# Performance work log

Hardware: AMD Instinct MI355X
Metric: run time of the kernel (lower is better)

Reference implementation:

```python
import jax, jax.numpy as jnp
from jax import lax
import numpy as np

TAPS = 4          # db2 filter length
LEVEL = 4
CH = 32
SLOPE = 10.0      # sigmoid sharpness of learned hard-threshold activation

# db2 decomposition low-pass coefficients (pywt convention)
_DB2 = np.array([-0.12940952255126037, 0.2241438680420134,
                 0.8365163037378079, 0.48296291314453416], dtype=np.float32)

def setup_inputs() -> dict:
    key = jax.random.key(0)
    k1, k2, k3 = jax.random.split(key, 3)
    x = jax.random.normal(k1, (128, CH, 4096), dtype=jnp.float32)
    # learned per-channel, per-level low-pass kernels: db2 init + small perturbation
    h_lo = jnp.asarray(_DB2)[None, None, :] + 0.02 * jax.random.normal(
        k2, (CH, LEVEL, TAPS), dtype=jnp.float32)
    # learned symmetric thresholds (Act_Init=0 -> small positive values)
    bias = 0.1 * jax.random.uniform(k3, (CH, LEVEL), dtype=jnp.float32)
    return {"x": x, "h_lo": h_lo, "bias": bias}

def _grouped_dwt_step(a, k_lo, k_hi):
    # a: [B,C,T]; kernels: [C,1,taps]; circular boundary, stride-2 downsample
    B, C, T = a.shape
    a_pad = jnp.concatenate([a, a[..., : TAPS - 1]], axis=-1)  # circular pad
    dn = ('NCH', 'OIH', 'NCH')
    lo = lax.conv_general_dilated(a_pad, k_lo, (2,), 'VALID',
                                  dimension_numbers=dn, feature_group_count=C)
    hi = lax.conv_general_dilated(a_pad, k_hi, (2,), 'VALID',
                                  dimension_numbers=dn, feature_group_count=C)
    return lo, hi  # each [B,C,T//2]

def reference(x, h_lo, bias):
    """Batched learned wavelet decomposition (all channels at once via grouped conv).
    Returns coefficients packed along last dim: [yl, d_L, ..., d_1] -> [B,C,T].
    """
    B, C, T = x.shape
    sign = ((-1.0) ** jnp.arange(TAPS)).astype(x.dtype)  # QMF sign flip
    a = x
    details = []
    for l in range(LEVEL):
        k_lo = h_lo[:, l, :][:, None, :]                       # [C,1,taps]
        k_hi = (sign * h_lo[:, l, ::-1])[:, None, :]           # high-pass via QMF
        a, hi = _grouped_dwt_step(a, k_lo, k_hi)
        b = bias[None, :, l, None]                             # [1,C,1]
        # symmetric sigmoid (soft hard-threshold) activation on detail coeffs
        d = hi * (jax.nn.sigmoid(SLOPE * (hi - b)) + jax.nn.sigmoid(-SLOPE * (hi + b)))
        details.append(d)
    # pack: approximation (coarsest) first, then details coarsest->finest
    return jnp.concatenate([a] + details[::-1], axis=-1)
```

## Files before the change

### kernel.cpp

```cpp
#include <hip/hip_runtime.h>
#include <math.h>

#define TLEN 4096
#define LEVELS 4
#define CHANS 32
#define SLOPE 10.0f

__device__ __forceinline__ float clamp30(float v) {
    return __builtin_amdgcn_fmed3f(v, -30.f, 30.f);
}

__device__ __forceinline__ float sgate(float hi, float b) {
    const float ea = __expf(clamp30(-SLOPE * (hi - b)));
    const float eb = __expf(clamp30( SLOPE * (hi + b)));
    return hi * (2.f + ea + eb) * __builtin_amdgcn_rcpf((1.f + ea) * (1.f + eb));
}

__global__ __launch_bounds__(256) void lwpt_kernel(
    const float* __restrict__ x, const float* __restrict__ h_lo,
    const float* __restrict__ bias, float* __restrict__ out)
{
    __shared__ float bufA[2048];
    __shared__ float bufB[1024];

    const int bc  = blockIdx.x;
    const int c   = bc & (CHANS - 1);
    const int tid = threadIdx.x;

    const float* xrow = x   + (size_t)bc * TLEN;
    float*       orow = out + (size_t)bc * TLEN;

    const float4 k0v = ((const float4*)h_lo)[c * LEVELS + 0];
    const float4 k1v = ((const float4*)h_lo)[c * LEVELS + 1];
    const float4 k2v = ((const float4*)h_lo)[c * LEVELS + 2];
    const float4 k3v = ((const float4*)h_lo)[c * LEVELS + 3];
    const float b0 = bias[c * LEVELS + 0];
    const float b1 = bias[c * LEVELS + 1];
    const float b2 = bias[c * LEVELS + 2];
    const float b3 = bias[c * LEVELS + 3];

    {
        const float4* x4 = (const float4*)xrow;
        float in[18];
        #pragma unroll
        for (int k = 0; k < 4; ++k) {
            const float4 v = x4[4 * tid + k];
            in[4*k+0] = v.x; in[4*k+1] = v.y; in[4*k+2] = v.z; in[4*k+3] = v.w;
        }
        const float2 e = *(const float2*)(xrow + ((16 * tid + 16) & (TLEN - 1)));
        in[16] = e.x; in[17] = e.y;

        float lo[8], dd[8];
        #pragma unroll
        for (int j = 0; j < 8; ++j) {
            const float a0 = in[2*j], a1 = in[2*j+1], a2 = in[2*j+2], a3 = in[2*j+3];
            lo[j] = a0*k0v.x + a1*k0v.y + a2*k0v.z + a3*k0v.w;
            const float hi = a0*k0v.w - a1*k0v.z + a2*k0v.y - a3*k0v.x;
            dd[j] = sgate(hi, b0);
        }
        ((float4*)bufA)[tid]          = make_float4(lo[0], lo[1], lo[2], lo[3]);
        ((float4*)(bufA + 1024))[tid] = make_float4(lo[4], lo[5], lo[6], lo[7]);
        float4* o4 = (float4*)(orow + 2048);
        o4[2*tid]   = make_float4(dd[0], dd[1], dd[2], dd[3]);
        o4[2*tid+1] = make_float4(dd[4], dd[5], dd[6], dd[7]);
    }
    __syncthreads();

    {
        float in[10];
        const float4 v0 = ((const float4*)bufA)[tid];
        const float4 v1 = ((const float4*)(bufA + 1024))[tid];
        in[0] = v0.x; in[1] = v0.y; in[2] = v0.z; in[3] = v0.w;
        in[4] = v1.x; in[5] = v1.y; in[6] = v1.z; in[7] = v1.w;
        const float2 e = *(const float2*)(bufA + ((4 * (tid + 1)) & 1023));
        in[8] = e.x; in[9] = e.y;

        float lo[4], dd[4];
        #pragma unroll
        for (int j = 0; j < 4; ++j) {
            const float a0 = in[2*j], a1 = in[2*j+1], a2 = in[2*j+2], a3 = in[2*j+3];
            lo[j] = a0*k1v.x + a1*k1v.y + a2*k1v.z + a3*k1v.w;
            const float hi = a0*k1v.w - a1*k1v.z + a2*k1v.y - a3*k1v.x;
            dd[j] = sgate(hi, b1);
        }
        ((float4*)bufB)[tid] = make_float4(lo[0], lo[1], lo[2], lo[3]);
        ((float4*)(orow + 1024))[tid] = make_float4(dd[0], dd[1], dd[2], dd[3]);
    }
    __syncthreads();

    {
        float in[6];
        const float4 v = ((const float4*)bufB)[tid];
        in[0] = v.x; in[1] = v.y; in[2] = v.z; in[3] = v.w;
        const float2 e = *(const float2*)(bufB + ((4 * tid + 4) & 1023));
        in[4] = e.x; in[5] = e.y;

        float lo[2], dd[2];
        #pragma unroll
        for (int j = 0; j < 2; ++j) {
            const float a0 = in[2*j], a1 = in[2*j+1], a2 = in[2*j+2], a3 = in[2*j+3];
            lo[j] = a0*k2v.x + a1*k2v.y + a2*k2v.z + a3*k2v.w;
            const float hi = a0*k2v.w - a1*k2v.z + a2*k2v.y - a3*k2v.x;
            dd[j] = sgate(hi, b2);
        }
        ((float2*)bufA)[tid] = make_float2(lo[0], lo[1]);
        ((float2*)(orow + 512))[tid] = make_float2(dd[0], dd[1]);
    }
    __syncthreads();

    {
        const float2 a01 = *(const float2*)(bufA + 2 * tid);
        const float2 e   = *(const float2*)(bufA + ((2 * tid + 2) & 511));
        const float a0 = a01.x, a1 = a01.y, a2 = e.x, a3 = e.y;
        const float lo = a0*k3v.x + a1*k3v.y + a2*k3v.z + a3*k3v.w;
        const float hi = a0*k3v.w - a1*k3v.z + a2*k3v.y - a3*k3v.x;
        orow[tid]       = lo;
        orow[256 + tid] = sgate(hi, b3);
    }
}

extern "C" void kernel_launch(void* const* d_in, const int* in_sizes, int n_in,
                              void* d_out, int out_size, void* d_ws, size_t ws_size,
                              hipStream_t stream) {
    const float* x    = (const float*)d_in[0];
    const float* h_lo = (const float*)d_in[1];
    const float* bias = (const float*)d_in[2];
    float* out = (float*)d_out;

    dim3 grid(128 * CHANS);
    dim3 block(256);
    lwpt_kernel<<<grid, block, 0, stream>>>(x, h_lo, bias, out);
}
```

Before: 26.29 us.

## Replace shared-memory level exchange with per-thread halo recomputation

Each thread now loads a wider input window (46 samples including a 30-sample halo) and computes all four wavelet levels entirely in registers. This removes the LDS buffers and the three block barriers between levels. In exchange it recomputes overlapping low-pass outputs (22 instead of 8 at level one, and so on), issues extra global loads that overlap with neighbouring threads, and raises register use.

Result: slower. 29.14 us (+10.8%).

```diff
diff --git a/kernel.cpp b/kernel.cpp
--- a/kernel.cpp
+++ b/kernel.cpp
@@ -20,9 +20,6 @@
     const float* __restrict__ x, const float* __restrict__ h_lo,
     const float* __restrict__ bias, float* __restrict__ out)
 {
-    __shared__ float bufA[2048];
-    __shared__ float bufB[1024];
-
     const int bc  = blockIdx.x;
     const int c   = bc & (CHANS - 1);
     const int tid = threadIdx.x;
@@ -39,81 +36,70 @@
     const float b2 = bias[c * LEVELS + 2];
     const float b3 = bias[c * LEVELS + 3];
 
+    float in[46];
+    const int base = 16 * tid;
+    #pragma unroll
+    for (int k = 0; k < 4; ++k) {
+        const float4 v = *(const float4*)(xrow + base + 4 * k);
+        in[4*k+0] = v.x; in[4*k+1] = v.y; in[4*k+2] = v.z; in[4*k+3] = v.w;
+    }
+    #pragma unroll
+    for (int k = 0; k < 7; ++k) {
+        const float4 v = *(const float4*)(xrow + ((base + 16 + 4 * k) & (TLEN - 1)));
+        in[16+4*k+0] = v.x; in[16+4*k+1] = v.y; in[16+4*k+2] = v.z; in[16+4*k+3] = v.w;
+    }
     {
-        const float4* x4 = (const float4*)xrow;
-        float in[18];
-        #pragma unroll
-        for (int k = 0; k < 4; ++k) {
-            const float4 v = x4[4 * tid + k];
-            in[4*k+0] = v.x; in[4*k+1] = v.y; in[4*k+2] = v.z; in[4*k+3] = v.w;
-        }
-        const float2 e = *(const float2*)(xrow + ((16 * tid + 16) & (TLEN - 1)));
-        in[16] = e.x; in[17] = e.y;
+        const float2 e = *(const float2*)(xrow + ((base + 44) & (TLEN - 1)));
+        in[44] = e.x; in[45] = e.y;
+    }
 
-        float lo[8], dd[8];
+    float lo1[22];
+    #pragma unroll
+    for (int j = 0; j < 22; ++j)
+        lo1[j] = in[2*j]*k0v.x + in[2*j+1]*k0v.y + in[2*j+2]*k0v.z + in[2*j+3]*k0v.w;
+    {
+        float dd[8];
         #pragma unroll
         for (int j = 0; j < 8; ++j) {
-            const float a0 = in[2*j], a1 = in[2*j+1], a2 = in[2*j+2], a3 = in[2*j+3];
-            lo[j] = a0*k0v.x + a1*k0v.y + a2*k0v.z + a3*k0v.w;
-            const float hi = a0*k0v.w - a1*k0v.z + a2*k0v.y - a3*k0v.x;
+            const float hi = in[2*j]*k0v.w - in[2*j+1]*k0v.z + in[2*j+2]*k0v.y - in[2*j+3]*k0v.x;
             dd[j] = sgate(hi, b0);
         }
-        ((float4*)bufA)[tid]          = make_float4(lo[0], lo[1], lo[2], lo[3]);
-        ((float4*)(bufA + 1024))[tid] = make_float4(lo[4], lo[5], lo[6], lo[7]);
         float4* o4 = (float4*)(orow + 2048);
         o4[2*tid]   = make_float4(dd[0], dd[1], dd[2], dd[3]);
         o4[2*tid+1] = make_float4(dd[4], dd[5], dd[6], dd[7]);
     }
-    __syncthreads();
+
+    float lo2[10];
+    #pragma unroll
+    for (int j = 0; j < 10; ++j)
+        lo2[j] = lo1[2*j]*k1v.x + lo1[2*j+1]*k1v.y + lo1[2*j+2]*k1v.z + lo1[2*j+3]*k1v.w;
+    {
+        float dd[4];
+        #pragma unroll
+        for (int j = 0; j < 4; ++j) {
+            const float hi = lo1[2*j]*k1v.w - lo1[2*j+1]*k1v.z + lo1[2*j+2]*k1v.y - lo1[2*j+3]*k1v.x;
+            dd[j] = sgate(hi, b1);
+        }
+        ((float4*)(orow + 1024))[tid] = make_float4(dd[0], dd[1], dd[2], dd[3]);
+    }
+
+    float lo3[4];
+    #pragma unroll
+    for (int j = 0; j < 4; ++j)
+        lo3[j] = lo2[2*j]*k2v.x + lo2[2*j+1]*k2v.y + lo2[2*j+2]*k2v.z + lo2[2*j+3]*k2v.w;
+    {
+        float dd[2];
+        #pragma unroll
+        for (int j = 0; j < 2; ++j) {
+            const float hi = lo2[2*j]*k2v.w - lo2[2*j+1]*k2v.z + lo2[2*j+2]*k2v.y - lo2[2*j+3]*k2v.x;
+            dd[j] = sgate(hi, b2);
+        }
+        ((float2*)(orow + 512))[tid] = make_float2(dd[0], dd[1]);
+    }
 
     {
-        float in[10];
-        const float4 v0 = ((const float4*)bufA)[tid];
-        const float4 v1 = ((const float4*)(bufA + 1024))[tid];
-        in[0] = v0.x; in[1] = v0.y; in[2] = v0.z; in[3] = v0.w;
-        in[4] = v1.x; in[5] = v1.y; in[6] = v1.z; in[7] = v1.w;
-        const float2 e = *(const float2*)(bufA + ((4 * (tid + 1)) & 1023));
-        in[8] = e.x; in[9] = e.y;
-
-        float lo[4], dd[4];
-        #pragma unroll
-        for (int j = 0; j < 4; ++j) {
-            const float a0 = in[2*j], a1 = in[2*j+1], a2 = in[2*j+2], a3 = in[2*j+3];
-            lo[j] = a0*k1v.x + a1*k1v.y + a2*k1v.z + a3*k1v.w;
-            const float hi = a0*k1v.w - a1*k1v.z + a2*k1v.y - a3*k1v.x;
-            dd[j] = sgate(hi, b1);
-        }
-        ((float4*)bufB)[tid] = make_float4(lo[0], lo[1], lo[2], lo[3]);
-        ((float4*)(orow + 1024))[tid] = make_float4(dd[0], dd[1], dd[2], dd[3]);
-    }
-    __syncthreads();
-
-    {
-        float in[6];
-        const float4 v = ((const float4*)bufB)[tid];
-        in[0] = v.x; in[1] = v.y; in[2] = v.z; in[3] = v.w;
-        const float2 e = *(const float2*)(bufB + ((4 * tid + 4) & 1023));
-        in[4] = e.x; in[5] = e.y;
-
-        float lo[2], dd[2];
-        #pragma unroll
-        for (int j = 0; j < 2; ++j) {
-            const float a0 = in[2*j], a1 = in[2*j+1], a2 = in[2*j+2], a3 = in[2*j+3];
-            lo[j] = a0*k2v.x + a1*k2v.y + a2*k2v.z + a3*k2v.w;
-            const float hi = a0*k2v.w - a1*k2v.z + a2*k2v.y - a3*k2v.x;
-            dd[j] = sgate(hi, b2);
-        }
-        ((float2*)bufA)[tid] = make_float2(lo[0], lo[1]);
-        ((float2*)(orow + 512))[tid] = make_float2(dd[0], dd[1]);
-    }
-    __syncthreads();
-
-    {
-        const float2 a01 = *(const float2*)(bufA + 2 * tid);
-        const float2 e   = *(const float2*)(bufA + ((2 * tid + 2) & 511));
-        const float a0 = a01.x, a1 = a01.y, a2 = e.x, a3 = e.y;
-        const float lo = a0*k3v.x + a1*k3v.y + a2*k3v.z + a3*k3v.w;
-        const float hi = a0*k3v.w - a1*k3v.z + a2*k3v.y - a3*k3v.x;
+        const float lo = lo3[0]*k3v.x + lo3[1]*k3v.y + lo3[2]*k3v.z + lo3[3]*k3v.w;
+        const float hi = lo3[0]*k3v.w - lo3[1]*k3v.z + lo3[2]*k3v.y - lo3[3]*k3v.x;
         orow[tid]       = lo;
         orow[256 + tid] = sgate(hi, b3);
     }
```

## Split each row across two blocks with halo recomputation

Applied to the files above, without the earlier changes.

Each (batch, channel) row is now handled by two 128-thread blocks, each covering half the time axis. The circular-boundary halo needed at each level is recomputed from the neighbouring half, using a few extra threads per level. This doubles the grid, shrinks shared memory per block and reduces the barrier scope, aiming for better occupancy and latency hiding. The cost is redundant halo reads and arithmetic, plus divergent branches in those threads.

Result: slower. 26.94 us (+2.5%).

```diff
diff --git a/kernel.cpp b/kernel.cpp
--- a/kernel.cpp
+++ b/kernel.cpp
@@ -16,14 +16,19 @@
     return hi * (2.f + ea + eb) * __builtin_amdgcn_rcpf((1.f + ea) * (1.f + eb));
 }
 
-__global__ __launch_bounds__(256) void lwpt_kernel(
+__global__ __launch_bounds__(128, 8) void lwpt_kernel(
     const float* __restrict__ x, const float* __restrict__ h_lo,
     const float* __restrict__ bias, float* __restrict__ out)
 {
-    __shared__ float bufA[2048];
-    __shared__ float bufB[1024];
+    __shared__ float smem[1560];
+    float* L1 = smem;
+    float* L2 = smem + 1040;
+    float* L3 = smem;
 
-    const int bc  = blockIdx.x;
+    const int bid = blockIdx.x;
+    const int bc  = bid >> 1;
+    const int hh  = bid & 1;
+    const int S   = hh << 11;
     const int c   = bc & (CHANS - 1);
     const int tid = threadIdx.x;
 
@@ -40,14 +45,14 @@
     const float b3 = bias[c * LEVELS + 3];
 
     {
-        const float4* x4 = (const float4*)xrow;
         float in[18];
+        const int base = S + 16 * tid;
         #pragma unroll
         for (int k = 0; k < 4; ++k) {
-            const float4 v = x4[4 * tid + k];
+            const float4 v = *(const float4*)(xrow + base + 4 * k);
             in[4*k+0] = v.x; in[4*k+1] = v.y; in[4*k+2] = v.z; in[4*k+3] = v.w;
         }
-        const float2 e = *(const float2*)(xrow + ((16 * tid + 16) & (TLEN - 1)));
+        const float2 e = *(const float2*)(xrow + ((base + 16) & (TLEN - 1)));
         in[16] = e.x; in[17] = e.y;
 
         float lo[8], dd[8];
@@ -58,64 +63,86 @@
             const float hi = a0*k0v.w - a1*k0v.z + a2*k0v.y - a3*k0v.x;
             dd[j] = sgate(hi, b0);
         }
-        ((float4*)bufA)[tid]          = make_float4(lo[0], lo[1], lo[2], lo[3]);
-        ((float4*)(bufA + 1024))[tid] = make_float4(lo[4], lo[5], lo[6], lo[7]);
-        float4* o4 = (float4*)(orow + 2048);
+        ((float4*)L1)[2*tid]   = make_float4(lo[0], lo[1], lo[2], lo[3]);
+        ((float4*)L1)[2*tid+1] = make_float4(lo[4], lo[5], lo[6], lo[7]);
+        float4* o4 = (float4*)(orow + 2048 + (S >> 1));
         o4[2*tid]   = make_float4(dd[0], dd[1], dd[2], dd[3]);
         o4[2*tid+1] = make_float4(dd[4], dd[5], dd[6], dd[7]);
+
+        if (tid >= 120 && tid < 127) {
+            const int s = tid - 120;
+            const int hb = S + 2048 + 4 * s;
+            const float4 v  = *(const float4*)(xrow + (hb & (TLEN - 1)));
+            const float2 e2 = *(const float2*)(xrow + ((hb + 4) & (TLEN - 1)));
+            L1[1024 + 2*s]     = v.x*k0v.x + v.y*k0v.y + v.z*k0v.z + v.w*k0v.w;
+            L1[1024 + 2*s + 1] = v.z*k0v.x + v.w*k0v.y + e2.x*k0v.z + e2.y*k0v.w;
+        }
     }
     __syncthreads();
 
     {
-        float in[10];
-        const float4 v0 = ((const float4*)bufA)[tid];
-        const float4 v1 = ((const float4*)(bufA + 1024))[tid];
-        in[0] = v0.x; in[1] = v0.y; in[2] = v0.z; in[3] = v0.w;
-        in[4] = v1.x; in[5] = v1.y; in[6] = v1.z; in[7] = v1.w;
-        const float2 e = *(const float2*)(bufA + ((4 * (tid + 1)) & 1023));
-        in[8] = e.x; in[9] = e.y;
+        const float4 v0 = *(const float4*)(L1 + 8*tid);
+        const float4 v1 = *(const float4*)(L1 + 8*tid + 4);
+        const float2 e  = *(const float2*)(L1 + 8*tid + 8);
+        float a[10];
+        a[0]=v0.x; a[1]=v0.y; a[2]=v0.z; a[3]=v0.w;
+        a[4]=v1.x; a[5]=v1.y; a[6]=v1.z; a[7]=v1.w;
+        a[8]=e.x;  a[9]=e.y;
 
         float lo[4], dd[4];
         #pragma unroll
         for (int j = 0; j < 4; ++j) {
-            const float a0 = in[2*j], a1 = in[2*j+1], a2 = in[2*j+2], a3 = in[2*j+3];
+            const float a0 = a[2*j], a1 = a[2*j+1], a2 = a[2*j+2], a3 = a[2*j+3];
             lo[j] = a0*k1v.x + a1*k1v.y + a2*k1v.z + a3*k1v.w;
             const float hi = a0*k1v.w - a1*k1v.z + a2*k1v.y - a3*k1v.x;
             dd[j] = sgate(hi, b1);
         }
-        ((float4*)bufB)[tid] = make_float4(lo[0], lo[1], lo[2], lo[3]);
-        ((float4*)(orow + 1024))[tid] = make_float4(dd[0], dd[1], dd[2], dd[3]);
+        ((float4*)L2)[tid] = make_float4(lo[0], lo[1], lo[2], lo[3]);
+        ((float4*)(orow + 1024 + (S >> 2)))[tid] = make_float4(dd[0], dd[1], dd[2], dd[3]);
+
+        if (tid >= 120 && tid < 126) {
+            const int s = tid - 120;
+            const float2 u0 = *(const float2*)(L1 + 1024 + 2*s);
+            const float2 u1 = *(const float2*)(L1 + 1024 + 2*s + 2);
+            L2[512 + s] = u0.x*k1v.x + u0.y*k1v.y + u1.x*k1v.z + u1.y*k1v.w;
+        }
     }
     __syncthreads();
 
     {
-        float in[6];
-        const float4 v = ((const float4*)bufB)[tid];
-        in[0] = v.x; in[1] = v.y; in[2] = v.z; in[3] = v.w;
-        const float2 e = *(const float2*)(bufB + ((4 * tid + 4) & 1023));
-        in[4] = e.x; in[5] = e.y;
+        const float4 v0 = *(const float4*)(L2 + 4*tid);
+        const float2 e  = *(const float2*)(L2 + 4*tid + 4);
+        float a[6];
+        a[0]=v0.x; a[1]=v0.y; a[2]=v0.z; a[3]=v0.w; a[4]=e.x; a[5]=e.y;
 
         float lo[2], dd[2];
         #pragma unroll
         for (int j = 0; j < 2; ++j) {
-            const float a0 = in[2*j], a1 = in[2*j+1], a2 = in[2*j+2], a3 = in[2*j+3];
+            const float a0 = a[2*j], a1 = a[2*j+1], a2 = a[2*j+2], a3 = a[2*j+3];
             lo[j] = a0*k2v.x + a1*k2v.y + a2*k2v.z + a3*k2v.w;
             const float hi = a0*k2v.w - a1*k2v.z + a2*k2v.y - a3*k2v.x;
             dd[j] = sgate(hi, b2);
         }
-        ((float2*)bufA)[tid] = make_float2(lo[0], lo[1]);
-        ((float2*)(orow + 512))[tid] = make_float2(dd[0], dd[1]);
+        ((float2*)L3)[tid] = make_float2(lo[0], lo[1]);
+        ((float2*)(orow + 512 + (S >> 3)))[tid] = make_float2(dd[0], dd[1]);
+
+        if (tid >= 120 && tid < 122) {
+            const int s = tid - 120;
+            const float2 u0 = *(const float2*)(L2 + 512 + 2*s);
+            const float2 u1 = *(const float2*)(L2 + 512 + 2*s + 2);
+            L3[256 + s] = u0.x*k2v.x + u0.y*k2v.y + u1.x*k2v.z + u1.y*k2v.w;
+        }
     }
     __syncthreads();
 
     {
-        const float2 a01 = *(const float2*)(bufA + 2 * tid);
-        const float2 e   = *(const float2*)(bufA + ((2 * tid + 2) & 511));
-        const float a0 = a01.x, a1 = a01.y, a2 = e.x, a3 = e.y;
+        const float2 a01 = *(const float2*)(L3 + 2*tid);
+        const float2 a23 = *(const float2*)(L3 + 2*tid + 2);
+        const float a0 = a01.x, a1 = a01.y, a2 = a23.x, a3 = a23.y;
         const float lo = a0*k3v.x + a1*k3v.y + a2*k3v.z + a3*k3v.w;
         const float hi = a0*k3v.w - a1*k3v.z + a2*k3v.y - a3*k3v.x;
-        orow[tid]       = lo;
-        orow[256 + tid] = sgate(hi, b3);
+        orow[(S >> 4) + tid]       = lo;
+        orow[256 + (S >> 4) + tid] = sgate(hi, b3);
     }
 }
 
@@ -127,7 +154,7 @@
     const float* bias = (const float*)d_in[2];
     float* out = (float*)d_out;
 
-    dim3 grid(128 * CHANS);
-    dim3 block(256);
+    dim3 grid(128 * CHANS * 2);
+    dim3 block(128);
     lwpt_kernel<<<grid, block, 0, stream>>>(x, h_lo, bias, out);
 }
```
